# Performance work log

Measured on AMD Instinct MI355X. Metric: run time of the kernel, lower is better.

The kernel has to match this reference:

```python
import jax, jax.numpy as jnp
import numpy as np

N, C, B = 800000, 64, 8
BN_EPS = 1e-5


def setup_inputs() -> dict:
    key = jax.random.key(0)
    ks = jax.random.split(key, 8)
    x = jax.random.normal(ks[0], (N, C), dtype=jnp.float32)
    # cumulative end-offsets of B equal segments: [100000, 200000, ..., 800000]
    o = (jnp.arange(1, B + 1, dtype=jnp.int64) * (N // B))
    s2 = 1.0 / np.sqrt(C)
    s1 = 1.0 / np.sqrt(2 * C)
    w2 = jax.random.uniform(ks[1], (C, C), jnp.float32, -s2, s2)      # linear2 Linear(C,C)
    b2 = jax.random.uniform(ks[2], (C,), jnp.float32, -s2, s2)
    w1 = jax.random.uniform(ks[3], (C, 2 * C), jnp.float32, -s1, s1)  # linear1 Linear(2C,C)
    b1 = jax.random.uniform(ks[4], (C,), jnp.float32, -s1, s1)
    gamma = jnp.ones((C,), jnp.float32)   # BatchNorm1d weight
    beta = jnp.zeros((C,), jnp.float32)   # BatchNorm1d bias
    return {"x": x, "o": o, "w2": w2, "b2": b2, "w1": w1, "b1": b1,
            "gamma": gamma, "beta": beta}


def reference(x, o, w2, b2, w1, b1, gamma, beta):
    n = x.shape[0]
    nb = o.shape[0]
    # segment id of each point: point i belongs to segment j iff o[j-1] <= i < o[j]
    seg = jnp.searchsorted(o, jnp.arange(n), side="right")          # [N]
    counts = jnp.diff(o, prepend=0).astype(x.dtype)                  # [B]
    # per-segment mean pool
    means = jax.ops.segment_sum(x, seg, num_segments=nb) / counts[:, None]  # [B, C]
    # linear2: Linear + ReLU on pooled vectors
    h = jax.nn.relu(means @ w2.T + b2)                               # [B, C]
    # broadcast pooled features back to points and concat
    cat = jnp.concatenate([x, h[seg]], axis=1)                       # [N, 2C]
    # linear1: Linear + BatchNorm1d (training-mode batch stats) + ReLU
    y = cat @ w1.T + b1                                              # [N, C]
    mu = y.mean(axis=0)
    var = y.var(axis=0)
    y = (y - mu) * jax.lax.rsqrt(var + BN_EPS) * gamma + beta
    return jax.nn.relu(y)
```

## Files before the change

kernel.cpp:

```cpp
#include <hip/hip_runtime.h>

#define NROWS 800000
#define SEGROWS 100000
#define K1_BLOCKS 800
#define K1_ROWS 1000

typedef __attribute__((ext_vector_type(8))) short bf16x8;
typedef __attribute__((ext_vector_type(4))) float f32x4;
typedef __attribute__((ext_vector_type(4))) short short4v;

__device__ inline unsigned short f2bf(float f) {
    unsigned u = __builtin_bit_cast(unsigned, f);
    return (unsigned short)((u + 0x7FFFu + ((u >> 16) & 1u)) >> 16);
}

__global__ void kzero(float* __restrict__ p) {
    int t = blockIdx.x * 256 + threadIdx.x;
    if (t < 4608) p[t] = 0.f;
}

__global__ __launch_bounds__(256, 2)
void k1_stats(const float* __restrict__ x, float* __restrict__ m2g, float* __restrict__ ssumg)
{
    __shared__ __align__(16) float smem[5120];
    short* xt = (short*)smem;
    const float4* X4 = (const float4*)x;
    int t = threadIdx.x, w = t >> 6, lane = t & 63;
    int c4 = t & 15, g = t >> 4;
    size_t r0 = (size_t)blockIdx.x * K1_ROWS;
    int seg = (int)(r0 / SEGROWS);

    f32x4 acc[4][4];
#pragma unroll
    for (int p = 0; p < 4; ++p)
#pragma unroll
        for (int q = 0; q < 4; ++q) acc[p][q] = (f32x4){0.f, 0.f, 0.f, 0.f};
    float s0 = 0, s1 = 0, s2 = 0, s3 = 0;

    for (int tile = 0; tile < K1_ROWS; tile += 128) {
        int nr = min(128, K1_ROWS - tile);
        __syncthreads();
#pragma unroll
        for (int h = 0; h < 2; ++h) {
            int rg = 8 * g + 4 * h;
            float4 v[4];
#pragma unroll
            for (int i = 0; i < 4; ++i) {
                int r = rg + i;
                if (r < nr) {
                    v[i] = X4[(r0 + tile + r) * 16 + c4];
                    s0 += v[i].x; s1 += v[i].y; s2 += v[i].z; s3 += v[i].w;
                } else v[i] = make_float4(0.f, 0.f, 0.f, 0.f);
            }
#pragma unroll
            for (int j = 0; j < 4; ++j) {
                short4v pk;
                pk[0] = (short)f2bf(((const float*)&v[0])[j]);
                pk[1] = (short)f2bf(((const float*)&v[1])[j]);
                pk[2] = (short)f2bf(((const float*)&v[2])[j]);
                pk[3] = (short)f2bf(((const float*)&v[3])[j]);
                *(short4v*)&xt[(4 * c4 + j) * 136 + rg] = pk;
            }
        }
        __syncthreads();
        bf16x8 f[4];
#pragma unroll
        for (int c0 = 0; c0 < 4; ++c0)
            f[c0] = *(const bf16x8*)&xt[(16 * c0 + (lane & 15)) * 136 + 32 * w + 8 * (lane >> 4)];
#pragma unroll
        for (int p = 0; p < 4; ++p)
#pragma unroll
            for (int q = 0; q < 4; ++q)
                acc[p][q] = __builtin_amdgcn_mfma_f32_16x16x32_bf16(f[p], f[q], acc[p][q], 0, 0, 0);
    }

    __syncthreads();
    ((float4*)(smem + 4096))[t] = make_float4(s0, s1, s2, s3);
    int qd = lane >> 4, cl = lane & 15;
    if (w == 0) {
#pragma unroll
        for (int p = 0; p < 4; ++p)
#pragma unroll
            for (int q = 0; q < 4; ++q)
#pragma unroll
                for (int i = 0; i < 4; ++i)
                    smem[(16 * p + 4 * qd + i) * 64 + 16 * q + cl] = acc[p][q][i];
    }
    __syncthreads();
    if (t < 64) {
        int cc4 = t >> 2, ii = t & 3;
        float s = 0;
#pragma unroll
        for (int u = 0; u < 16; ++u) s += smem[4096 + 4 * (cc4 + 16 * u) + ii];
        atomicAdd(&ssumg[seg * 64 + t], s);
    }
    for (int ww = 1; ww < 4; ++ww) {
        if (w == ww) {
#pragma unroll
            for (int p = 0; p < 4; ++p)
#pragma unroll
                for (int q = 0; q < 4; ++q)
#pragma unroll
                    for (int i = 0; i < 4; ++i)
                        smem[(16 * p + 4 * qd + i) * 64 + 16 * q + cl] += acc[p][q][i];
        }
        __syncthreads();
    }
    for (int f2 = t; f2 < 4096; f2 += 256) atomicAdd(&m2g[f2], smem[f2]);
}

__global__ __launch_bounds__(256)
void k2b_solve(const int* __restrict__ o,
               const float* __restrict__ w2, const float* __restrict__ b2,
               const float* __restrict__ w1, const float* __restrict__ b1,
               const float* __restrict__ gamma, const float* __restrict__ beta,
               const float* __restrict__ m2, const float* __restrict__ ssum,
               unsigned short* __restrict__ wpb, float* __restrict__ tbout)
{
    __shared__ float means[512], hb[512], cv[512], Sx[64], cnts[8], muS[64], sS[64], q1p[256];
    int t = threadIdx.x;
    if (t < 8) cnts[t] = (float)(o[t] - (t ? o[t - 1] : 0));
    __syncthreads();
    for (int i = t; i < 512; i += 256) means[i] = ssum[i] / cnts[i >> 6];
    __syncthreads();
    int c = t & 63, g = t >> 6;
    for (int b = g; b < 8; b += 4) {
        float a = b2[c];
        for (int k = 0; k < 64; ++k) a = fmaf(means[b * 64 + k], w2[c * 64 + k], a);
        hb[b * 64 + c] = fmaxf(a, 0.f);
    }
    __syncthreads();
    for (int b = g; b < 8; b += 4) {
        float a = b1[c];
        for (int k = 0; k < 64; ++k) a = fmaf(hb[b * 64 + k], w1[c * 128 + 64 + k], a);
        cv[b * 64 + c] = a;
    }
    __syncthreads();
    if (t < 64) {
        float s = 0;
        for (int b = 0; b < 8; ++b) s += ssum[b * 64 + t];
        Sx[t] = s;
    }
    __syncthreads();
    {
        float p = 0;
        for (int j = g * 16; j < g * 16 + 16; ++j) {
            float vj = 0;
            for (int k = 0; k < 64; ++k) vj = fmaf(w1[c * 128 + k], m2[j * 64 + k], vj);
            p = fmaf(w1[c * 128 + j], vj, p);
        }
        q1p[g * 64 + c] = p;
    }
    __syncthreads();
    if (t < 64) {
        const float Nf = (float)NROWS;
        float mu = 0;
        for (int k = 0; k < 64; ++k) mu = fmaf(w1[t * 128 + k], Sx[k], mu);
        float q2 = 0, q3 = 0, msum = 0;
        for (int b = 0; b < 8; ++b) {
            float gv = cv[b * 64 + t];
            msum += cnts[b] * gv;
            q3 = fmaf(cnts[b] * gv, gv, q3);
            float dot = 0;
            for (int k = 0; k < 64; ++k) dot = fmaf(w1[t * 128 + k], ssum[b * 64 + k], dot);
            q2 = fmaf(2.f * gv, dot, q2);
        }
        mu = (mu + msum) / Nf;
        float q1 = q1p[t] + q1p[64 + t] + q1p[128 + t] + q1p[192 + t];
        float var = (q1 + q2 + q3) / Nf - mu * mu;
        float s = gamma[t] * rsqrtf(var + 1e-5f);
        muS[t] = mu; sS[t] = s;
    }
    __syncthreads();
    for (int f = t; f < 4096; f += 256)
        wpb[f] = f2bf(w1[(f >> 6) * 128 + (f & 63)] * sS[f >> 6]);
    for (int f = t; f < 512; f += 256)
        tbout[f] = (cv[f] - muS[f & 63]) * sS[f & 63] + beta[f & 63];
}

__global__ __launch_bounds__(256, 3)
void k3_gemm(const float* __restrict__ x, const unsigned short* __restrict__ wpb,
             const float* __restrict__ tb, float* __restrict__ out)
{
    __shared__ __align__(16) short bt[64 * 72];
    __shared__ float tbs[512];
    int t = threadIdx.x, lane = t & 63, w = t >> 6;
    size_t r0 = (size_t)blockIdx.x * 256;

    for (int f = t; f < 512; f += 256) {
        int c = f >> 3, kg = f & 7;
        uint4 vv = ((const uint4*)wpb)[f];
        *(uint4*)&bt[c * 72 + kg * 8] = vv;
    }
    for (int f = t; f < 512; f += 256) tbs[f] = tb[f];
    __syncthreads();

    int cl = lane & 15, qd = lane >> 4;
    bf16x8 B[4][2];
#pragma unroll
    for (int n = 0; n < 4; ++n)
#pragma unroll
        for (int k0 = 0; k0 < 2; ++k0)
            B[n][k0] = *(const bf16x8*)&bt[(16 * n + cl) * 72 + 32 * k0 + 8 * qd];

    int rbase = (int)r0 + 64 * w;
    f32x4 acc[4][4];
#pragma unroll
    for (int m = 0; m < 4; ++m)
#pragma unroll
        for (int n = 0; n < 4; ++n) acc[m][n] = (f32x4){0.f, 0.f, 0.f, 0.f};

#pragma unroll
    for (int m = 0; m < 4; ++m) {
        const float* rp = x + (size_t)(rbase + 16 * m + cl) * 64 + 8 * qd;
        float4 u0 = *(const float4*)(rp);
        float4 u1 = *(const float4*)(rp + 4);
        float4 u2 = *(const float4*)(rp + 32);
        float4 u3 = *(const float4*)(rp + 36);
        bf16x8 A0, A1;
        A0[0] = (short)f2bf(u0.x); A0[1] = (short)f2bf(u0.y);
        A0[2] = (short)f2bf(u0.z); A0[3] = (short)f2bf(u0.w);
        A0[4] = (short)f2bf(u1.x); A0[5] = (short)f2bf(u1.y);
        A0[6] = (short)f2bf(u1.z); A0[7] = (short)f2bf(u1.w);
        A1[0] = (short)f2bf(u2.x); A1[1] = (short)f2bf(u2.y);
        A1[2] = (short)f2bf(u2.z); A1[3] = (short)f2bf(u2.w);
        A1[4] = (short)f2bf(u3.x); A1[5] = (short)f2bf(u3.y);
        A1[6] = (short)f2bf(u3.z); A1[7] = (short)f2bf(u3.w);
#pragma unroll
        for (int n = 0; n < 4; ++n) {
            acc[m][n] = __builtin_amdgcn_mfma_f32_16x16x32_bf16(A0, B[n][0], acc[m][n], 0, 0, 0);
            acc[m][n] = __builtin_amdgcn_mfma_f32_16x16x32_bf16(A1, B[n][1], acc[m][n], 0, 0, 0);
        }
    }

    int seg0 = rbase / SEGROWS;
    int bnd = (seg0 + 1) * SEGROWS;
    int seg1 = min(seg0 + 1, 7);
    float tA[4], tB[4];
#pragma unroll
    for (int n = 0; n < 4; ++n) {
        tA[n] = tbs[seg0 * 64 + 16 * n + cl];
        tB[n] = tbs[seg1 * 64 + 16 * n + cl];
    }
#pragma unroll
    for (int m = 0; m < 4; ++m)
#pragma unroll
        for (int i = 0; i < 4; ++i) {
            int grow = rbase + 16 * m + 4 * qd + i;
            bool hi = grow >= bnd;
#pragma unroll
            for (int n = 0; n < 4; ++n) {
                float tv = hi ? tB[n] : tA[n];
                float vv = fmaxf(acc[m][n][i] + tv, 0.f);
                out[(size_t)grow * 64 + 16 * n + cl] = vv;
            }
        }
}

extern "C" void kernel_launch(void* const* d_in, const int* in_sizes, int n_in,
                              void* d_out, int out_size, void* d_ws, size_t ws_size,
                              hipStream_t stream)
{
    const float* x  = (const float*)d_in[0];
    const int*   o  = (const int*)d_in[1];
    const float* w2 = (const float*)d_in[2];
    const float* b2 = (const float*)d_in[3];
    const float* w1 = (const float*)d_in[4];
    const float* b1 = (const float*)d_in[5];
    const float* gm = (const float*)d_in[6];
    const float* bt = (const float*)d_in[7];
    float* out = (float*)d_out;
    float* ws  = (float*)d_ws;

    float*          m2g  = ws;
    float*          ssum = ws + 4096;
    float*          tbv  = ws + 4608;
    unsigned short* wpb  = (unsigned short*)(ws + 5120);

    kzero<<<18, 256, 0, stream>>>(ws);
    k1_stats<<<K1_BLOCKS, 256, 0, stream>>>(x, m2g, ssum);
    k2b_solve<<<1, 256, 0, stream>>>(o, w2, b2, w1, b1, gm, bt, m2g, ssum, wpb, tbv);
    k3_gemm<<<3125, 256, 0, stream>>>(x, wpb, tbv, out);
}
```

Measured before the change: 474.5 us.

## Fuse stats, solve, and GEMM into one cooperative persistent kernel

Replaces the four launches (zero, stats, solve, GEMM) with a single cooperative kernel of 256 persistent blocks, separated by grid.sync barriers. Per-block Gram and column sums now go to a partials buffer and are reduced deterministically after a barrier, instead of through global atomics. This removes launch gaps, the zeroing kernel and atomic contention. In exchange, block 0 runs the solve alone while all other blocks wait, and the GEMM phase loses occupancy, using grid-stride tiles with 2 blocks per CU instead of 3.

```diff
diff --git a/kernel.cpp b/kernel.cpp
--- a/kernel.cpp
+++ b/kernel.cpp
@@ -1,9 +1,15 @@
 #include <hip/hip_runtime.h>
+#include <hip/hip_cooperative_groups.h>
+
+namespace cg = cooperative_groups;
 
 #define NROWS 800000
 #define SEGROWS 100000
-#define K1_BLOCKS 800
-#define K1_ROWS 1000
+#define NBLK 256
+#define RPB 3125
+#define NTILES 3125
+#define PART_BASE 8192
+#define PART_STRIDE 4160
 
 typedef __attribute__((ext_vector_type(8))) short bf16x8;
 typedef __attribute__((ext_vector_type(4))) float f32x4;
@@ -14,247 +20,270 @@
     return (unsigned short)((u + 0x7FFFu + ((u >> 16) & 1u)) >> 16);
 }
 
-__global__ void kzero(float* __restrict__ p) {
-    int t = blockIdx.x * 256 + threadIdx.x;
-    if (t < 4608) p[t] = 0.f;
-}
-
 __global__ __launch_bounds__(256, 2)
-void k1_stats(const float* __restrict__ x, float* __restrict__ m2g, float* __restrict__ ssumg)
+void kfused(const float* __restrict__ x, const int* __restrict__ o,
+            const float* __restrict__ w2, const float* __restrict__ b2,
+            const float* __restrict__ w1, const float* __restrict__ b1,
+            const float* __restrict__ gamma, const float* __restrict__ beta,
+            float* __restrict__ out, float* __restrict__ ws)
 {
     __shared__ __align__(16) float smem[5120];
-    short* xt = (short*)smem;
-    const float4* X4 = (const float4*)x;
-    int t = threadIdx.x, w = t >> 6, lane = t & 63;
-    int c4 = t & 15, g = t >> 4;
-    size_t r0 = (size_t)blockIdx.x * K1_ROWS;
-    int seg = (int)(r0 / SEGROWS);
-
-    f32x4 acc[4][4];
-#pragma unroll
-    for (int p = 0; p < 4; ++p)
-#pragma unroll
-        for (int q = 0; q < 4; ++q) acc[p][q] = (f32x4){0.f, 0.f, 0.f, 0.f};
-    float s0 = 0, s1 = 0, s2 = 0, s3 = 0;
-
-    for (int tile = 0; tile < K1_ROWS; tile += 128) {
-        int nr = min(128, K1_ROWS - tile);
-        __syncthreads();
-#pragma unroll
-        for (int h = 0; h < 2; ++h) {
-            int rg = 8 * g + 4 * h;
-            float4 v[4];
-#pragma unroll
-            for (int i = 0; i < 4; ++i) {
-                int r = rg + i;
-                if (r < nr) {
-                    v[i] = X4[(r0 + tile + r) * 16 + c4];
-                    s0 += v[i].x; s1 += v[i].y; s2 += v[i].z; s3 += v[i].w;
-                } else v[i] = make_float4(0.f, 0.f, 0.f, 0.f);
-            }
-#pragma unroll
-            for (int j = 0; j < 4; ++j) {
-                short4v pk;
-                pk[0] = (short)f2bf(((const float*)&v[0])[j]);
-                pk[1] = (short)f2bf(((const float*)&v[1])[j]);
-                pk[2] = (short)f2bf(((const float*)&v[2])[j]);
-                pk[3] = (short)f2bf(((const float*)&v[3])[j]);
-                *(short4v*)&xt[(4 * c4 + j) * 136 + rg] = pk;
-            }
-        }
-        __syncthreads();
-        bf16x8 f[4];
-#pragma unroll
-        for (int c0 = 0; c0 < 4; ++c0)
-            f[c0] = *(const bf16x8*)&xt[(16 * c0 + (lane & 15)) * 136 + 32 * w + 8 * (lane >> 4)];
+    cg::grid_group grid = cg::this_grid();
+    const int t = threadIdx.x, b = blockIdx.x;
+    const int w = t >> 6, lane = t & 63;
+    const int c4 = t & 15, g = t >> 4;
+    const int cl = lane & 15, qd = lane >> 4;
+
+    float* m2   = ws;
+    float* ssum = ws + 4096;
+    float* tb   = ws + 4608;
+    unsigned short* wpb = (unsigned short*)(ws + 5120);
+    float* part = ws + PART_BASE;
+
+    {
+        short* xt = (short*)smem;
+        const float4* X4 = (const float4*)x;
+        size_t r0 = (size_t)b * RPB;
+
+        f32x4 acc[4][4];
 #pragma unroll
         for (int p = 0; p < 4; ++p)
 #pragma unroll
-            for (int q = 0; q < 4; ++q)
-                acc[p][q] = __builtin_amdgcn_mfma_f32_16x16x32_bf16(f[p], f[q], acc[p][q], 0, 0, 0);
+            for (int q = 0; q < 4; ++q) acc[p][q] = (f32x4){0.f, 0.f, 0.f, 0.f};
+        float s0 = 0, s1 = 0, s2 = 0, s3 = 0;
+
+        for (int tile = 0; tile < RPB; tile += 128) {
+            int nr = min(128, RPB - tile);
+            __syncthreads();
+#pragma unroll
+            for (int h = 0; h < 2; ++h) {
+                int rg = 8 * g + 4 * h;
+                float4 v[4];
+#pragma unroll
+                for (int i = 0; i < 4; ++i) {
+                    int r = rg + i;
+                    if (r < nr) {
+                        v[i] = X4[(r0 + tile + r) * 16 + c4];
+                        s0 += v[i].x; s1 += v[i].y; s2 += v[i].z; s3 += v[i].w;
+                    } else v[i] = make_float4(0.f, 0.f, 0.f, 0.f);
+                }
+#pragma unroll
+                for (int j = 0; j < 4; ++j) {
+                    short4v pk;
+                    pk[0] = (short)f2bf(((const float*)&v[0])[j]);
+                    pk[1] = (short)f2bf(((const float*)&v[1])[j]);
+                    pk[2] = (short)f2bf(((const float*)&v[2])[j]);
+                    pk[3] = (short)f2bf(((const float*)&v[3])[j]);
+                    *(short4v*)&xt[(4 * c4 + j) * 136 + rg] = pk;
+                }
+            }
+            __syncthreads();
+            bf16x8 f[4];
+#pragma unroll
+            for (int c0 = 0; c0 < 4; ++c0)
+                f[c0] = *(const bf16x8*)&xt[(16 * c0 + cl) * 136 + 32 * w + 8 * qd];
+#pragma unroll
+            for (int p = 0; p < 4; ++p)
+#pragma unroll
+                for (int q = 0; q < 4; ++q)
+                    acc[p][q] = __builtin_amdgcn_mfma_f32_16x16x32_bf16(f[p], f[q], acc[p][q], 0, 0, 0);
+        }
+
+        __syncthreads();
+        ((float4*)(smem + 4096))[t] = make_float4(s0, s1, s2, s3);
+        if (w == 0) {
+#pragma unroll
+            for (int p = 0; p < 4; ++p)
+#pragma unroll
+                for (int q = 0; q < 4; ++q)
+#pragma unroll
+                    for (int i = 0; i < 4; ++i)
+                        smem[(16 * p + 4 * qd + i) * 64 + 16 * q + cl] = acc[p][q][i];
+        }
+        __syncthreads();
+        for (int ww = 1; ww < 4; ++ww) {
+            if (w == ww) {
+#pragma unroll
+                for (int p = 0; p < 4; ++p)
+#pragma unroll
+                    for (int q = 0; q < 4; ++q)
+#pragma unroll
+                        for (int i = 0; i < 4; ++i)
+                            smem[(16 * p + 4 * qd + i) * 64 + 16 * q + cl] += acc[p][q][i];
+            }
+            __syncthreads();
+        }
+        if (t < 64) {
+            float s = 0;
+#pragma unroll
+            for (int u = 0; u < 16; ++u) s += smem[4096 + 4 * ((t >> 2) + 16 * u) + (t & 3)];
+            part[(size_t)b * PART_STRIDE + 4096 + t] = s;
+        }
+        for (int f2 = t; f2 < 4096; f2 += 256)
+            part[(size_t)b * PART_STRIDE + f2] = smem[f2];
     }
-
-    __syncthreads();
-    ((float4*)(smem + 4096))[t] = make_float4(s0, s1, s2, s3);
-    int qd = lane >> 4, cl = lane & 15;
-    if (w == 0) {
-#pragma unroll
-        for (int p = 0; p < 4; ++p)
-#pragma unroll
-            for (int q = 0; q < 4; ++q)
-#pragma unroll
-                for (int i = 0; i < 4; ++i)
-                    smem[(16 * p + 4 * qd + i) * 64 + 16 * q + cl] = acc[p][q][i];
+    __threadfence();
+    grid.sync();
+
+    if (b < 16) {
+        int e = b * 256 + t;
+        float s = 0;
+#pragma unroll 4
+        for (int i = 0; i < NBLK; ++i) s += part[(size_t)i * PART_STRIDE + e];
+        m2[e] = s;
+    } else if (b < 18) {
+        int idx = (b - 16) * 256 + t;
+        int sg = idx >> 6, c = idx & 63;
+        float s = 0;
+#pragma unroll 4
+        for (int i = 0; i < 32; ++i) s += part[(size_t)(sg * 32 + i) * PART_STRIDE + 4096 + c];
+        ssum[idx] = s;
     }
-    __syncthreads();
-    if (t < 64) {
-        int cc4 = t >> 2, ii = t & 3;
-        float s = 0;
-#pragma unroll
-        for (int u = 0; u < 16; ++u) s += smem[4096 + 4 * (cc4 + 16 * u) + ii];
-        atomicAdd(&ssumg[seg * 64 + t], s);
+    __threadfence();
+    grid.sync();
+
+    if (b == 0) {
+        float* means = smem;
+        float* hb    = smem + 512;
+        float* cv    = smem + 1024;
+        float* Sx    = smem + 1536;
+        float* cnts  = smem + 1600;
+        float* muS   = smem + 1608;
+        float* sS    = smem + 1672;
+        float* q1p   = smem + 1736;
+        if (t < 8) cnts[t] = (float)(o[t] - (t ? o[t - 1] : 0));
+        __syncthreads();
+        for (int i = t; i < 512; i += 256) means[i] = ssum[i] / cnts[i >> 6];
+        __syncthreads();
+        int c = t & 63, gq = t >> 6;
+        for (int bb = gq; bb < 8; bb += 4) {
+            float a = b2[c];
+            for (int k = 0; k < 64; ++k) a = fmaf(means[bb * 64 + k], w2[c * 64 + k], a);
+            hb[bb * 64 + c] = fmaxf(a, 0.f);
+        }
+        __syncthreads();
+        for (int bb = gq; bb < 8; bb += 4) {
+            float a = b1[c];
+            for (int k = 0; k < 64; ++k) a = fmaf(hb[bb * 64 + k], w1[c * 128 + 64 + k], a);
+            cv[bb * 64 + c] = a;
+        }
+        __syncthreads();
+        if (t < 64) {
+            float s = 0;
+            for (int bb = 0; bb < 8; ++bb) s += ssum[bb * 64 + t];
+            Sx[t] = s;
+        }
+        __syncthreads();
+        {
+            float p = 0;
+            for (int j = gq * 16; j < gq * 16 + 16; ++j) {
+                float vj = 0;
+                for (int k = 0; k < 64; ++k) vj = fmaf(w1[c * 128 + k], m2[j * 64 + k], vj);
+                p = fmaf(w1[c * 128 + j], vj, p);
+            }
+            q1p[gq * 64 + c] = p;
+        }
+        __syncthreads();
+        if (t < 64) {
+            const float Nf = (float)NROWS;
+            float mu = 0;
+            for (int k = 0; k < 64; ++k) mu = fmaf(w1[t * 128 + k], Sx[k], mu);
+            float q2 = 0, q3 = 0, msum = 0;
+            for (int bb = 0; bb < 8; ++bb) {
+                float gv = cv[bb * 64 + t];
+                msum += cnts[bb] * gv;
+                q3 = fmaf(cnts[bb] * gv, gv, q3);
+                float dot = 0;
+                for (int k = 0; k < 64; ++k) dot = fmaf(w1[t * 128 + k], ssum[bb * 64 + k], dot);
+                q2 = fmaf(2.f * gv, dot, q2);
+            }
+            mu = (mu + msum) / Nf;
+            float q1 = q1p[t] + q1p[64 + t] + q1p[128 + t] + q1p[192 + t];
+            float var = (q1 + q2 + q3) / Nf - mu * mu;
+            float s = gamma[t] * rsqrtf(var + 1e-5f);
+            muS[t] = mu; sS[t] = s;
+        }
+        __syncthreads();
+        for (int f = t; f < 4096; f += 256)
+            wpb[f] = f2bf(w1[(f >> 6) * 128 + (f & 63)] * sS[f >> 6]);
+        for (int f = t; f < 512; f += 256)
+            tb[f] = (cv[f] - muS[f & 63]) * sS[f & 63] + beta[f & 63];
     }
-    for (int ww = 1; ww < 4; ++ww) {
-        if (w == ww) {
-#pragma unroll
-            for (int p = 0; p < 4; ++p)
-#pragma unroll
-                for (int q = 0; q < 4; ++q)
-#pragma unroll
-                    for (int i = 0; i < 4; ++i)
-                        smem[(16 * p + 4 * qd + i) * 64 + 16 * q + cl] += acc[p][q][i];
-        }
-        __syncthreads();
+    __threadfence();
+    grid.sync();
+
+    {
+        short* bt  = (short*)smem;
+        float* tbs = smem + 2304;
+        for (int f = t; f < 512; f += 256) {
+            uint4 vv = ((const uint4*)wpb)[f];
+            *(uint4*)&bt[(f >> 3) * 72 + (f & 7) * 8] = vv;
+        }
+        for (int f = t; f < 512; f += 256) tbs[f] = tb[f];
+        __syncthreads();
+
+        bf16x8 B[4][2];
+#pragma unroll
+        for (int n = 0; n < 4; ++n)
+#pragma unroll
+            for (int k0 = 0; k0 < 2; ++k0)
+                B[n][k0] = *(const bf16x8*)&bt[(16 * n + cl) * 72 + 32 * k0 + 8 * qd];
+
+        for (int tt = b; tt < NTILES; tt += NBLK) {
+            int rbase = tt * 256 + 64 * w;
+            f32x4 acc[4][4];
+#pragma unroll
+            for (int m = 0; m < 4; ++m)
+#pragma unroll
+                for (int n = 0; n < 4; ++n) acc[m][n] = (f32x4){0.f, 0.f, 0.f, 0.f};
+
+#pragma unroll
+            for (int m = 0; m < 4; ++m) {
+                const float* rp = x + (size_t)(rbase + 16 * m + cl) * 64 + 8 * qd;
+                float4 u0 = *(const float4*)(rp);
+                float4 u1 = *(const float4*)(rp + 4);
+                float4 u2 = *(const float4*)(rp + 32);
+                float4 u3 = *(const float4*)(rp + 36);
+                bf16x8 A0, A1;
+                A0[0] = (short)f2bf(u0.x); A0[1] = (short)f2bf(u0.y);
+                A0[2] = (short)f2bf(u0.z); A0[3] = (short)f2bf(u0.w);
+                A0[4] = (short)f2bf(u1.x); A0[5] = (short)f2bf(u1.y);
+                A0[6] = (short)f2bf(u1.z); A0[7] = (short)f2bf(u1.w);
+                A1[0] = (short)f2bf(u2.x); A1[1] = (short)f2bf(u2.y);
+                A1[2] = (short)f2bf(u2.z); A1[3] = (short)f2bf(u2.w);
+                A1[4] = (short)f2bf(u3.x); A1[5] = (short)f2bf(u3.y);
+                A1[6] = (short)f2bf(u3.z); A1[7] = (short)f2bf(u3.w);
+#pragma unroll
+                for (int n = 0; n < 4; ++n) {
+                    acc[m][n] = __builtin_amdgcn_mfma_f32_16x16x32_bf16(A0, B[n][0], acc[m][n], 0, 0, 0);
+                    acc[m][n] = __builtin_amdgcn_mfma_f32_16x16x32_bf16(A1, B[n][1], acc[m][n], 0, 0, 0);
+                }
+            }
+
+            int seg0 = rbase / SEGROWS;
+            int bnd = (seg0 + 1) * SEGROWS;
+            int seg1 = min(seg0 + 1, 7);
+            float tA[4], tB[4];
+#pragma unroll
+            for (int n = 0; n < 4; ++n) {
+                tA[n] = tbs[seg0 * 64 + 16 * n + cl];
+                tB[n] = tbs[seg1 * 64 + 16 * n + cl];
+            }
+#pragma unroll
+            for (int m = 0; m < 4; ++m)
+#pragma unroll
+                for (int i = 0; i < 4; ++i) {
+                    int grow = rbase + 16 * m + 4 * qd + i;
+                    bool hi = grow >= bnd;
+#pragma unroll
+                    for (int n = 0; n < 4; ++n) {
+                        float tv = hi ? tB[n] : tA[n];
+                        float vv = fmaxf(acc[m][n][i] + tv, 0.f);
+                        out[(size_t)grow * 64 + 16 * n + cl] = vv;
+                    }
+                }
+        }
     }
-    for (int f2 = t; f2 < 4096; f2 += 256) atomicAdd(&m2g[f2], smem[f2]);
-}
-
-__global__ __launch_bounds__(256)
-void k2b_solve(const int* __restrict__ o,
-               const float* __restrict__ w2, const float* __restrict__ b2,
-               const float* __restrict__ w1, const float* __restrict__ b1,
-               const float* __restrict__ gamma, const float* __restrict__ beta,
-               const float* __restrict__ m2, const float* __restrict__ ssum,
-               unsigned short* __restrict__ wpb, float* __restrict__ tbout)
-{
-    __shared__ float means[512], hb[512], cv[512], Sx[64], cnts[8], muS[64], sS[64], q1p[256];
-    int t = threadIdx.x;
-    if (t < 8) cnts[t] = (float)(o[t] - (t ? o[t - 1] : 0));
-    __syncthreads();
-    for (int i = t; i < 512; i += 256) means[i] = ssum[i] / cnts[i >> 6];
-    __syncthreads();
-    int c = t & 63, g = t >> 6;
-    for (int b = g; b < 8; b += 4) {
-        float a = b2[c];
-        for (int k = 0; k < 64; ++k) a = fmaf(means[b * 64 + k], w2[c * 64 + k], a);
-        hb[b * 64 + c] = fmaxf(a, 0.f);
-    }
-    __syncthreads();
-    for (int b = g; b < 8; b += 4) {
-        float a = b1[c];
-        for (int k = 0; k < 64; ++k) a = fmaf(hb[b * 64 + k], w1[c * 128 + 64 + k], a);
-        cv[b * 64 + c] = a;
-    }
-    __syncthreads();
-    if (t < 64) {
-        float s = 0;
-        for (int b = 0; b < 8; ++b) s += ssum[b * 64 + t];
-        Sx[t] = s;
-    }
-    __syncthreads();
-    {
-        float p = 0;
-        for (int j = g * 16; j < g * 16 + 16; ++j) {
-            float vj = 0;
-            for (int k = 0; k < 64; ++k) vj = fmaf(w1[c * 128 + k], m2[j * 64 + k], vj);
-            p = fmaf(w1[c * 128 + j], vj, p);
-        }
-        q1p[g * 64 + c] = p;
-    }
-    __syncthreads();
-    if (t < 64) {
-        const float Nf = (float)NROWS;
-        float mu = 0;
-        for (int k = 0; k < 64; ++k) mu = fmaf(w1[t * 128 + k], Sx[k], mu);
-        float q2 = 0, q3 = 0, msum = 0;
-        for (int b = 0; b < 8; ++b) {
-            float gv = cv[b * 64 + t];
-            msum += cnts[b] * gv;
-            q3 = fmaf(cnts[b] * gv, gv, q3);
-            float dot = 0;
-            for (int k = 0; k < 64; ++k) dot = fmaf(w1[t * 128 + k], ssum[b * 64 + k], dot);
-            q2 = fmaf(2.f * gv, dot, q2);
-        }
-        mu = (mu + msum) / Nf;
-        float q1 = q1p[t] + q1p[64 + t] + q1p[128 + t] + q1p[192 + t];
-        float var = (q1 + q2 + q3) / Nf - mu * mu;
-        float s = gamma[t] * rsqrtf(var + 1e-5f);
-        muS[t] = mu; sS[t] = s;
-    }
-    __syncthreads();
-    for (int f = t; f < 4096; f += 256)
-        wpb[f] = f2bf(w1[(f >> 6) * 128 + (f & 63)] * sS[f >> 6]);
-    for (int f = t; f < 512; f += 256)
-        tbout[f] = (cv[f] - muS[f & 63]) * sS[f & 63] + beta[f & 63];
-}
-
-__global__ __launch_bounds__(256, 3)
-void k3_gemm(const float* __restrict__ x, const unsigned short* __restrict__ wpb,
-             const float* __restrict__ tb, float* __restrict__ out)
-{
-    __shared__ __align__(16) short bt[64 * 72];
-    __shared__ float tbs[512];
-    int t = threadIdx.x, lane = t & 63, w = t >> 6;
-    size_t r0 = (size_t)blockIdx.x * 256;
-
-    for (int f = t; f < 512; f += 256) {
-        int c = f >> 3, kg = f & 7;
-        uint4 vv = ((const uint4*)wpb)[f];
-        *(uint4*)&bt[c * 72 + kg * 8] = vv;
-    }
-    for (int f = t; f < 512; f += 256) tbs[f] = tb[f];
-    __syncthreads();
-
-    int cl = lane & 15, qd = lane >> 4;
-    bf16x8 B[4][2];
-#pragma unroll
-    for (int n = 0; n < 4; ++n)
-#pragma unroll
-        for (int k0 = 0; k0 < 2; ++k0)
-            B[n][k0] = *(const bf16x8*)&bt[(16 * n + cl) * 72 + 32 * k0 + 8 * qd];
-
-    int rbase = (int)r0 + 64 * w;
-    f32x4 acc[4][4];
-#pragma unroll
-    for (int m = 0; m < 4; ++m)
-#pragma unroll
-        for (int n = 0; n < 4; ++n) acc[m][n] = (f32x4){0.f, 0.f, 0.f, 0.f};
-
-#pragma unroll
-    for (int m = 0; m < 4; ++m) {
-        const float* rp = x + (size_t)(rbase + 16 * m + cl) * 64 + 8 * qd;
-        float4 u0 = *(const float4*)(rp);
-        float4 u1 = *(const float4*)(rp + 4);
-        float4 u2 = *(const float4*)(rp + 32);
-        float4 u3 = *(const float4*)(rp + 36);
-        bf16x8 A0, A1;
-        A0[0] = (short)f2bf(u0.x); A0[1] = (short)f2bf(u0.y);
-        A0[2] = (short)f2bf(u0.z); A0[3] = (short)f2bf(u0.w);
-        A0[4] = (short)f2bf(u1.x); A0[5] = (short)f2bf(u1.y);
-        A0[6] = (short)f2bf(u1.z); A0[7] = (short)f2bf(u1.w);
-        A1[0] = (short)f2bf(u2.x); A1[1] = (short)f2bf(u2.y);
-        A1[2] = (short)f2bf(u2.z); A1[3] = (short)f2bf(u2.w);
-        A1[4] = (short)f2bf(u3.x); A1[5] = (short)f2bf(u3.y);
-        A1[6] = (short)f2bf(u3.z); A1[7] = (short)f2bf(u3.w);
-#pragma unroll
-        for (int n = 0; n < 4; ++n) {
-            acc[m][n] = __builtin_amdgcn_mfma_f32_16x16x32_bf16(A0, B[n][0], acc[m][n], 0, 0, 0);
-            acc[m][n] = __builtin_amdgcn_mfma_f32_16x16x32_bf16(A1, B[n][1], acc[m][n], 0, 0, 0);
-        }
-    }
-
-    int seg0 = rbase / SEGROWS;
-    int bnd = (seg0 + 1) * SEGROWS;
-    int seg1 = min(seg0 + 1, 7);
-    float tA[4], tB[4];
-#pragma unroll
-    for (int n = 0; n < 4; ++n) {
-        tA[n] = tbs[seg0 * 64 + 16 * n + cl];
-        tB[n] = tbs[seg1 * 64 + 16 * n + cl];
-    }
-#pragma unroll
-    for (int m = 0; m < 4; ++m)
-#pragma unroll
-        for (int i = 0; i < 4; ++i) {
-            int grow = rbase + 16 * m + 4 * qd + i;
-            bool hi = grow >= bnd;
-#pragma unroll
-            for (int n = 0; n < 4; ++n) {
-                float tv = hi ? tB[n] : tA[n];
-                float vv = fmaxf(acc[m][n][i] + tv, 0.f);
-                out[(size_t)grow * 64 + 16 * n + cl] = vv;
-            }
-        }
 }
 
 extern "C" void kernel_launch(void* const* d_in, const int* in_sizes, int n_in,
@@ -272,13 +301,7 @@
     float* out = (float*)d_out;
     float* ws  = (float*)d_ws;
 
-    float*          m2g  = ws;
-    float*          ssum = ws + 4096;
-    float*          tbv  = ws + 4608;
-    unsigned short* wpb  = (unsigned short*)(ws + 5120);
-
-    kzero<<<18, 256, 0, stream>>>(ws);
-    k1_stats<<<K1_BLOCKS, 256, 0, stream>>>(x, m2g, ssum);
-    k2b_solve<<<1, 256, 0, stream>>>(o, w2, b2, w1, b1, gm, bt, m2g, ssum, wpb, tbv);
-    k3_gemm<<<3125, 256, 0, stream>>>(x, wpb, tbv, out);
+    void* args[] = {(void*)&x, (void*)&o, (void*)&w2, (void*)&b2, (void*)&w1,
+                    (void*)&b1, (void*)&gm, (void*)&bt, (void*)&out, (void*)&ws};
+    hipLaunchCooperativeKernel((void*)kfused, dim3(NBLK), dim3(256), args, 0, stream);
 }
```

After: 704.3 us. +48.4%, slower.

## Cache bf16 copy of x in stats pass, replace atomics with partial reduce

Applied to the files above, without the earlier changes.

The stats kernel now writes a bf16 copy of x to workspace, so the GEMM pass reads half the bytes instead of re-reading fp32 x and converting it again. Global atomics and the zeroing kernel are replaced by per-block partial buffers plus a separate reduction kernel. The GEMM is transposed so each lane stores contiguous float4 outputs, and occupancy hints are raised. The cost is an extra ~100MB bf16 write in the first pass and an extra kernel launch.

```diff
diff --git a/kernel.cpp b/kernel.cpp
--- a/kernel.cpp
+++ b/kernel.cpp
@@ -4,6 +4,10 @@
 #define SEGROWS 100000
 #define K1_BLOCKS 800
 #define K1_ROWS 1000
+#define NTILES 3125
+#define PART_BASE 8192
+#define PART_STRIDE 4160
+#define XB_BASE (PART_BASE + K1_BLOCKS * PART_STRIDE)
 
 typedef __attribute__((ext_vector_type(8))) short bf16x8;
 typedef __attribute__((ext_vector_type(4))) float f32x4;
@@ -14,21 +18,17 @@
     return (unsigned short)((u + 0x7FFFu + ((u >> 16) & 1u)) >> 16);
 }
 
-__global__ void kzero(float* __restrict__ p) {
-    int t = blockIdx.x * 256 + threadIdx.x;
-    if (t < 4608) p[t] = 0.f;
-}
-
-__global__ __launch_bounds__(256, 2)
-void k1_stats(const float* __restrict__ x, float* __restrict__ m2g, float* __restrict__ ssumg)
+__global__ __launch_bounds__(256, 3)
+void k1_stats(const float* __restrict__ x, float* __restrict__ part,
+              unsigned short* __restrict__ xb)
 {
     __shared__ __align__(16) float smem[5120];
     short* xt = (short*)smem;
     const float4* X4 = (const float4*)x;
     int t = threadIdx.x, w = t >> 6, lane = t & 63;
     int c4 = t & 15, g = t >> 4;
+    int cl = lane & 15, qd = lane >> 4;
     size_t r0 = (size_t)blockIdx.x * K1_ROWS;
-    int seg = (int)(r0 / SEGROWS);
 
     f32x4 acc[4][4];
 #pragma unroll
@@ -52,21 +52,33 @@
                     s0 += v[i].x; s1 += v[i].y; s2 += v[i].z; s3 += v[i].w;
                 } else v[i] = make_float4(0.f, 0.f, 0.f, 0.f);
             }
+            unsigned short bf[4][4];
+#pragma unroll
+            for (int i = 0; i < 4; ++i) {
+                bf[i][0] = f2bf(v[i].x); bf[i][1] = f2bf(v[i].y);
+                bf[i][2] = f2bf(v[i].z); bf[i][3] = f2bf(v[i].w);
+            }
 #pragma unroll
             for (int j = 0; j < 4; ++j) {
                 short4v pk;
-                pk[0] = (short)f2bf(((const float*)&v[0])[j]);
-                pk[1] = (short)f2bf(((const float*)&v[1])[j]);
-                pk[2] = (short)f2bf(((const float*)&v[2])[j]);
-                pk[3] = (short)f2bf(((const float*)&v[3])[j]);
+                pk[0] = (short)bf[0][j]; pk[1] = (short)bf[1][j];
+                pk[2] = (short)bf[2][j]; pk[3] = (short)bf[3][j];
                 *(short4v*)&xt[(4 * c4 + j) * 136 + rg] = pk;
+            }
+#pragma unroll
+            for (int i = 0; i < 4; ++i) {
+                int r = rg + i;
+                if (r < nr) {
+                    unsigned short u4[4] = {bf[i][0], bf[i][1], bf[i][2], bf[i][3]};
+                    *(uint2*)&xb[(r0 + tile + r) * 64 + 4 * c4] = *(const uint2*)u4;
+                }
             }
         }
         __syncthreads();
         bf16x8 f[4];
 #pragma unroll
         for (int c0 = 0; c0 < 4; ++c0)
-            f[c0] = *(const bf16x8*)&xt[(16 * c0 + (lane & 15)) * 136 + 32 * w + 8 * (lane >> 4)];
+            f[c0] = *(const bf16x8*)&xt[(16 * c0 + cl) * 136 + 32 * w + 8 * qd];
 #pragma unroll
         for (int p = 0; p < 4; ++p)
 #pragma unroll
@@ -76,7 +88,6 @@
 
     __syncthreads();
     ((float4*)(smem + 4096))[t] = make_float4(s0, s1, s2, s3);
-    int qd = lane >> 4, cl = lane & 15;
     if (w == 0) {
 #pragma unroll
         for (int p = 0; p < 4; ++p)
@@ -87,13 +98,6 @@
                     smem[(16 * p + 4 * qd + i) * 64 + 16 * q + cl] = acc[p][q][i];
     }
     __syncthreads();
-    if (t < 64) {
-        int cc4 = t >> 2, ii = t & 3;
-        float s = 0;
-#pragma unroll
-        for (int u = 0; u < 16; ++u) s += smem[4096 + 4 * (cc4 + 16 * u) + ii];
-        atomicAdd(&ssumg[seg * 64 + t], s);
-    }
     for (int ww = 1; ww < 4; ++ww) {
         if (w == ww) {
 #pragma unroll
@@ -106,7 +110,35 @@
         }
         __syncthreads();
     }
-    for (int f2 = t; f2 < 4096; f2 += 256) atomicAdd(&m2g[f2], smem[f2]);
+    if (t < 64) {
+        float s = 0;
+#pragma unroll
+        for (int u = 0; u < 16; ++u) s += smem[4096 + 4 * ((t >> 2) + 16 * u) + (t & 3)];
+        part[(size_t)blockIdx.x * PART_STRIDE + 4096 + t] = s;
+    }
+    for (int f2 = t; f2 < 4096; f2 += 256)
+        part[(size_t)blockIdx.x * PART_STRIDE + f2] = smem[f2];
+}
+
+__global__ __launch_bounds__(256)
+void k2a_reduce(const float* __restrict__ part, float* __restrict__ m2,
+                float* __restrict__ ssum)
+{
+    int t = threadIdx.x, b = blockIdx.x;
+    if (b < 16) {
+        int e = b * 256 + t;
+        float s = 0;
+#pragma unroll 8
+        for (int i = 0; i < K1_BLOCKS; ++i) s += part[(size_t)i * PART_STRIDE + e];
+        m2[e] = s;
+    } else {
+        int idx = (b - 16) * 256 + t;
+        int sg = idx >> 6, c = idx & 63;
+        float s = 0;
+#pragma unroll 8
+        for (int i = 0; i < 100; ++i) s += part[(size_t)(sg * 100 + i) * PART_STRIDE + 4096 + c];
+        ssum[idx] = s;
+    }
 }
 
 __global__ __launch_bounds__(256)
@@ -178,83 +210,57 @@
         tbout[f] = (cv[f] - muS[f & 63]) * sS[f & 63] + beta[f & 63];
 }
 
-__global__ __launch_bounds__(256, 3)
-void k3_gemm(const float* __restrict__ x, const unsigned short* __restrict__ wpb,
+__global__ __launch_bounds__(256, 4)
+void k3_gemm(const unsigned short* __restrict__ xb, const unsigned short* __restrict__ wpb,
              const float* __restrict__ tb, float* __restrict__ out)
 {
     __shared__ __align__(16) short bt[64 * 72];
-    __shared__ float tbs[512];
+    __shared__ __align__(16) float tbs[512];
     int t = threadIdx.x, lane = t & 63, w = t >> 6;
+    int cl = lane & 15, qd = lane >> 4;
     size_t r0 = (size_t)blockIdx.x * 256;
 
     for (int f = t; f < 512; f += 256) {
-        int c = f >> 3, kg = f & 7;
         uint4 vv = ((const uint4*)wpb)[f];
-        *(uint4*)&bt[c * 72 + kg * 8] = vv;
+        *(uint4*)&bt[(f >> 3) * 72 + (f & 7) * 8] = vv;
     }
     for (int f = t; f < 512; f += 256) tbs[f] = tb[f];
     __syncthreads();
 
-    int cl = lane & 15, qd = lane >> 4;
-    bf16x8 B[4][2];
-#pragma unroll
-    for (int n = 0; n < 4; ++n)
-#pragma unroll
-        for (int k0 = 0; k0 < 2; ++k0)
-            B[n][k0] = *(const bf16x8*)&bt[(16 * n + cl) * 72 + 32 * k0 + 8 * qd];
+    bf16x8 Wf[4][2];
+#pragma unroll
+    for (int p = 0; p < 4; ++p)
+#pragma unroll
+        for (int kh = 0; kh < 2; ++kh)
+            Wf[p][kh] = *(const bf16x8*)&bt[(16 * p + cl) * 72 + 32 * kh + 8 * qd];
 
     int rbase = (int)r0 + 64 * w;
-    f32x4 acc[4][4];
-#pragma unroll
-    for (int m = 0; m < 4; ++m)
-#pragma unroll
-        for (int n = 0; n < 4; ++n) acc[m][n] = (f32x4){0.f, 0.f, 0.f, 0.f};
-
-#pragma unroll
-    for (int m = 0; m < 4; ++m) {
-        const float* rp = x + (size_t)(rbase + 16 * m + cl) * 64 + 8 * qd;
-        float4 u0 = *(const float4*)(rp);
-        float4 u1 = *(const float4*)(rp + 4);
-        float4 u2 = *(const float4*)(rp + 32);
-        float4 u3 = *(const float4*)(rp + 36);
-        bf16x8 A0, A1;
-        A0[0] = (short)f2bf(u0.x); A0[1] = (short)f2bf(u0.y);
-        A0[2] = (short)f2bf(u0.z); A0[3] = (short)f2bf(u0.w);
-        A0[4] = (short)f2bf(u1.x); A0[5] = (short)f2bf(u1.y);
-        A0[6] = (short)f2bf(u1.z); A0[7] = (short)f2bf(u1.w);
-        A1[0] = (short)f2bf(u2.x); A1[1] = (short)f2bf(u2.y);
-        A1[2] = (short)f2bf(u2.z); A1[3] = (short)f2bf(u2.w);
-        A1[4] = (short)f2bf(u3.x); A1[5] = (short)f2bf(u3.y);
-        A1[6] = (short)f2bf(u3.z); A1[7] = (short)f2bf(u3.w);
-#pragma unroll
-        for (int n = 0; n < 4; ++n) {
-            acc[m][n] = __builtin_amdgcn_mfma_f32_16x16x32_bf16(A0, B[n][0], acc[m][n], 0, 0, 0);
-            acc[m][n] = __builtin_amdgcn_mfma_f32_16x16x32_bf16(A1, B[n][1], acc[m][n], 0, 0, 0);
-        }
-    }
-
-    int seg0 = rbase / SEGROWS;
-    int bnd = (seg0 + 1) * SEGROWS;
-    int seg1 = min(seg0 + 1, 7);
-    float tA[4], tB[4];
-#pragma unroll
-    for (int n = 0; n < 4; ++n) {
-        tA[n] = tbs[seg0 * 64 + 16 * n + cl];
-        tB[n] = tbs[seg1 * 64 + 16 * n + cl];
-    }
-#pragma unroll
-    for (int m = 0; m < 4; ++m)
-#pragma unroll
-        for (int i = 0; i < 4; ++i) {
-            int grow = rbase + 16 * m + 4 * qd + i;
-            bool hi = grow >= bnd;
-#pragma unroll
-            for (int n = 0; n < 4; ++n) {
-                float tv = hi ? tB[n] : tA[n];
-                float vv = fmaxf(acc[m][n][i] + tv, 0.f);
-                out[(size_t)grow * 64 + 16 * n + cl] = vv;
-            }
-        }
+#pragma unroll
+    for (int rt = 0; rt < 4; ++rt) {
+        int row16 = rbase + 16 * rt;
+        int r = row16 + cl;
+        const bf16x8 B0 = *(const bf16x8*)&xb[(size_t)r * 64 + 8 * qd];
+        const bf16x8 B1 = *(const bf16x8*)&xb[(size_t)r * 64 + 32 + 8 * qd];
+        int sg = r / SEGROWS;
+        f32x4 acc[4];
+#pragma unroll
+        for (int p = 0; p < 4; ++p) acc[p] = (f32x4){0.f, 0.f, 0.f, 0.f};
+#pragma unroll
+        for (int p = 0; p < 4; ++p) {
+            acc[p] = __builtin_amdgcn_mfma_f32_16x16x32_bf16(Wf[p][0], B0, acc[p], 0, 0, 0);
+            acc[p] = __builtin_amdgcn_mfma_f32_16x16x32_bf16(Wf[p][1], B1, acc[p], 0, 0, 0);
+        }
+#pragma unroll
+        for (int p = 0; p < 4; ++p) {
+            f32x4 tv = *(const f32x4*)&tbs[sg * 64 + 16 * p + 4 * qd];
+            float4 res;
+            res.x = fmaxf(acc[p][0] + tv[0], 0.f);
+            res.y = fmaxf(acc[p][1] + tv[1], 0.f);
+            res.z = fmaxf(acc[p][2] + tv[2], 0.f);
+            res.w = fmaxf(acc[p][3] + tv[3], 0.f);
+            *(float4*)&out[(size_t)r * 64 + 16 * p + 4 * qd] = res;
+        }
+    }
 }
 
 extern "C" void kernel_launch(void* const* d_in, const int* in_sizes, int n_in,
@@ -276,9 +282,11 @@
     float*          ssum = ws + 4096;
     float*          tbv  = ws + 4608;
     unsigned short* wpb  = (unsigned short*)(ws + 5120);
-
-    kzero<<<18, 256, 0, stream>>>(ws);
-    k1_stats<<<K1_BLOCKS, 256, 0, stream>>>(x, m2g, ssum);
+    float*          part = ws + PART_BASE;
+    unsigned short* xb   = (unsigned short*)(ws + XB_BASE);
+
+    k1_stats<<<K1_BLOCKS, 256, 0, stream>>>(x, part, xb);
+    k2a_reduce<<<18, 256, 0, stream>>>(part, m2g, ssum);
     k2b_solve<<<1, 256, 0, stream>>>(o, w2, b2, w1, b1, gm, bt, m2g, ssum, wpb, tbv);
-    k3_gemm<<<3125, 256, 0, stream>>>(x, wpb, tbv, out);
-}
+    k3_gemm<<<NTILES, 256, 0, stream>>>(xb, wpb, tbv, out);
+}
```

After: 513.6 us. 8.2% more time.
